# Kernel tuning notes

Hardware: AMD Instinct MI355X
Metric: run time of the kernel (lower is better)

The kernel has to match this reference:

```python
import jax, jax.numpy as jnp
import numpy as np
from jax import lax

B, C, H, W = 4, 192, 64, 64
D_STATE, D_CONV, EXPAND = 16, 4, 2.0
DI = int(EXPAND * C)           # 384 inner dim
DT_RANK = (C + 15) // 16       # 12
EPS = 1e-5


def setup_inputs() -> dict:
    key = jax.random.key(0)
    ks = jax.random.split(key, 16)
    r = lambda k, shp, s=0.02: jax.random.normal(k, shp, jnp.float32) * s
    inp = {
        'x': jax.random.normal(ks[0], (B, C, H, W), jnp.float32),
        'ln_w': jnp.ones((C,), jnp.float32),
        'ln_b': jnp.zeros((C,), jnp.float32),
        'in_proj_w': r(ks[1], (2 * DI, C)),
        'conv_w': r(ks[2], (DI, 1, D_CONV), 0.1),
        'conv_b': jnp.zeros((DI,), jnp.float32),
        'x_proj_w': r(ks[3], (DT_RANK + 2 * D_STATE, DI)),
        'dt_proj_w': r(ks[4], (DI, DT_RANK), 0.1),
        'dt_proj_b': jnp.full((DI,), -4.0, jnp.float32),  # softplus -> small dt
        'A_log': jnp.log(jnp.broadcast_to(jnp.arange(1, D_STATE + 1, dtype=jnp.float32), (DI, D_STATE))),
        'D': jnp.ones((DI,), jnp.float32),
        'out_proj_w': r(ks[5], (C, DI)),
        'rf_w': r(ks[6], (C, C, 3, 3), 0.05),
        'rf_b': jnp.zeros((C,), jnp.float32),
        'bn_w': jnp.ones((C,), jnp.float32),
        'bn_b': jnp.zeros((C,), jnp.float32),
        'bn_mean': jnp.zeros((C,), jnp.float32),
        'bn_var': jnp.ones((C,), jnp.float32),
    }
    return inp


def _selective_scan(delta, A, Bc, Cc, u):
    # delta,u: (B,L,DI); Bc,Cc: (B,L,N); A: (DI,N)
    def step(h, xs):
        d_t, b_t, c_t, u_t = xs  # (B,DI),(B,N),(B,N),(B,DI)
        dA = jnp.exp(d_t[:, :, None] * A[None])            # (B,DI,N)
        h = dA * h + (d_t * u_t)[:, :, None] * b_t[:, None, :]
        y = jnp.einsum('bdn,bn->bd', h, c_t)
        return h, y
    h0 = jnp.zeros((delta.shape[0], A.shape[0], A.shape[1]), delta.dtype)
    xs = (delta.swapaxes(0, 1), Bc.swapaxes(0, 1), Cc.swapaxes(0, 1), u.swapaxes(0, 1))
    _, ys = lax.scan(step, h0, xs)
    return ys.swapaxes(0, 1)  # (B,L,DI)


def _forward(x, ln_w, ln_b, in_proj_w, conv_w, conv_b, x_proj_w, dt_proj_w,
             dt_proj_b, A_log, D, out_proj_w, rf_w, rf_b, bn_w, bn_b, bn_mean, bn_var):
    b, c, h, w = x.shape
    L = h * w
    t = x.reshape(b, c, L).transpose(0, 2, 1)              # (B,L,C) tokens
    res = t
    mu = t.mean(-1, keepdims=True)
    var = t.var(-1, keepdims=True)
    tn = (t - mu) * lax.rsqrt(var + EPS) * ln_w + ln_b
    xz = jnp.einsum('blc,ec->ble', tn, in_proj_w)          # (B,L,2*DI)
    xi, z = jnp.split(xz, 2, axis=-1)
    # causal depthwise conv1d over L
    xi = xi.transpose(0, 2, 1)                             # (B,DI,L)
    xi = lax.conv_general_dilated(xi, conv_w, (1,), [(D_CONV - 1, 0)],
                                  feature_group_count=DI,
                                  dimension_numbers=('NCH', 'OIH', 'NCH'))
    xi = jax.nn.silu(xi + conv_b[None, :, None])
    xt = xi.transpose(0, 2, 1)                             # (B,L,DI)
    dbl = jnp.einsum('bld,ed->ble', xt, x_proj_w)
    dt, Bc, Cc = jnp.split(dbl, [DT_RANK, DT_RANK + D_STATE], axis=-1)
    delta = jax.nn.softplus(jnp.einsum('blr,dr->bld', dt, dt_proj_w) + dt_proj_b)
    A = -jnp.exp(A_log)
    y = _selective_scan(delta, A, Bc, Cc, xt) + xt * D
    y = y * jax.nn.silu(z)
    t = res + jnp.einsum('bld,cd->blc', y, out_proj_w)     # residual
    x2 = t.transpose(0, 2, 1).reshape(b, c, h, w)
    # refine: conv3x3 + BN(eval) + ReLU
    x2 = lax.conv_general_dilated(x2, rf_w, (1, 1), 'SAME',
                                  dimension_numbers=('NCHW', 'OIHW', 'NCHW'))
    x2 = x2 + rf_b[None, :, None, None]
    x2 = (x2 - bn_mean[None, :, None, None]) * lax.rsqrt(bn_var + EPS)[None, :, None, None]
    x2 = x2 * bn_w[None, :, None, None] + bn_b[None, :, None, None]
    return jax.nn.relu(x2)


def reference(x, ln_w, ln_b, in_proj_w, conv_w, conv_b, x_proj_w, dt_proj_w,
              dt_proj_b, A_log, D, out_proj_w, rf_w, rf_b, bn_w, bn_b, bn_mean, bn_var):
    return _forward(x, ln_w, ln_b, in_proj_w, conv_w, conv_b, x_proj_w, dt_proj_w,
                    dt_proj_b, A_log, D, out_proj_w, rf_w, rf_b, bn_w, bn_b,
                    bn_mean, bn_var)
```

## Files before the change

### kernel.cpp

```cpp
#include <hip/hip_runtime.h>


#define Bn 4
#define Cn 192
#define Hn 64
#define Wn 64
#define Ln 4096
#define DIn 384
#define Nst 16
#define RK 12
#define E2 768
#define NCn 64
#define EPSf 1e-5f
#define HP 66
#define HP2 4356

typedef __bf16 bf16x8 __attribute__((ext_vector_type(8)));
typedef float f32x4 __attribute__((ext_vector_type(4)));
typedef unsigned short u16;
typedef unsigned int u32;

static __device__ __forceinline__ float sigmoidf_(float v) {
    return 1.f / (1.f + __expf(-v));
}
static __device__ __forceinline__ float softplusf_(float v) {
    return v > 15.f ? v : __logf(1.f + __expf(v));
}
static __device__ __forceinline__ u16 f2bf(float f) {
    u32 u = __float_as_uint(f);
    u32 r = (u + 0x7FFFu + ((u >> 16) & 1u)) >> 16;
    return (u16)r;
}
static __device__ __forceinline__ float bf2f(u16 v) {
    return __uint_as_float(((u32)v) << 16);
}
static __device__ __forceinline__ float fexp2(float x) {
#if __has_builtin(__builtin_amdgcn_exp2f)
    return __builtin_amdgcn_exp2f(x);
#else
    return __expf(x * 0.69314718056f);
#endif
}
static __device__ __forceinline__ float quad_sum_dpp(float p) {
    float t, r;
    asm volatile("v_add_f32 %0, %1, %1 quad_perm:[1,0,3,2] row_mask:0xf bank_mask:0xf"
                 : "=&v"(t) : "v"(p));
    asm volatile("v_add_f32 %0, %1, %1 quad_perm:[2,3,0,1] row_mask:0xf bank_mask:0xf"
                 : "=&v"(r) : "v"(t));
    return r;
}
static __device__ __forceinline__ void async16(const u16* g, u16* l) {
    __builtin_amdgcn_global_load_lds((__attribute__((address_space(1))) void*)g,
                                     (__attribute__((address_space(3))) void*)l, 16, 0, 0);
}

__global__ __launch_bounds__(256) void k_prep(const float* __restrict__ rfw,
                                              const float* __restrict__ xpw,
                                              const float* __restrict__ dtw,
                                              const float* __restrict__ inpw,
                                              const float* __restrict__ Wo,
                                              const float* __restrict__ rfb,
                                              const float* __restrict__ bnw,
                                              const float* __restrict__ bnb,
                                              const float* __restrict__ bnm,
                                              const float* __restrict__ bnv,
                                              u16* __restrict__ wcv2,
                                              u16* __restrict__ wcomb_bf,
                                              u16* __restrict__ inpw_bf,
                                              u16* __restrict__ wo_bf,
                                              float* __restrict__ scsf,
                                              u16* __restrict__ t2pad) {
    int g = blockIdx.x * 256 + threadIdx.x;
    if (g < 331776) {
        int co = g / 1728;
        int rem = g - co * 1728;
        int tap = rem / Cn, ci = rem - tap * Cn;
        wcv2[g] = f2bf(rfw[((size_t)co * Cn + ci) * 9 + tap]);
    } else if (g < 503808) {
        int i = g - 331776;
        int row = i / 384, k = i - row * 384;
        float v = 0.f;
        if (row < 384) {
#pragma unroll
            for (int r = 0; r < RK; ++r)
                v = fmaf(dtw[row * RK + r], xpw[r * 384 + k], v);
        } else if (row < 416) {
            v = xpw[(RK + row - 384) * 384 + k];
        }
        wcomb_bf[i] = f2bf(v);
    } else if (g < 651264) {
        int i = g - 503808;
        inpw_bf[i] = f2bf(inpw[i]);
    } else if (g < 724992) {
        int i = g - 651264;
        wo_bf[i] = f2bf(Wo[i]);
    } else if (g < 725376) {
        int i = g - 724992;
        if (i < 192) {
            scsf[i] = bnw[i] * rsqrtf(bnv[i] + EPSf);
        } else {
            int c = i - 192;
            float sc = bnw[c] * rsqrtf(bnv[c] + EPSf);
            scsf[i] = (rfb[c] - bnm[c]) * sc + bnb[c];
        }
    } else if (g < 750336) {
        int i = g - 725376;
        int chunk = i % 24;
        int pos = i / 24;
        int b = pos / 260;
        int p = pos - b * 260;
        int cell;
        if (p < 66) cell = p;
        else if (p < 132) cell = 65 * HP + (p - 66);
        else if (p < 196) cell = (p - 132 + 1) * HP;
        else cell = (p - 196 + 1) * HP + 65;
        *(uint4*)&t2pad[((size_t)b * HP2 + cell) * Cn + chunk * 8] = make_uint4(0u, 0u, 0u, 0u);
    }
}

__global__ __launch_bounds__(256) void k_ln(const float* __restrict__ x,
                                            const float* __restrict__ lnw,
                                            const float* __restrict__ lnb,
                                            u16* __restrict__ tn_bf) {
    __shared__ float tile[Cn][65];
    __shared__ float red[2][4][64];
    __shared__ float mean_s[64], rstd_s[64];
    int b = blockIdx.x >> 6;
    int l0 = (blockIdx.x & 63) << 6;
    int tid = threadIdx.x;
    for (int idx = tid; idx < Cn * 64; idx += 256) {
        int c = idx >> 6, ll = idx & 63;
        tile[c][ll] = x[((size_t)(b * Cn + c) << 12) + l0 + ll];
    }
    __syncthreads();
    int ll = tid & 63, grp = tid >> 6;
    float s = 0.f, s2 = 0.f;
    for (int c = grp * 48; c < grp * 48 + 48; ++c) {
        float v = tile[c][ll];
        s += v; s2 += v * v;
    }
    red[0][grp][ll] = s; red[1][grp][ll] = s2;
    __syncthreads();
    if (tid < 64) {
        float m = red[0][0][tid] + red[0][1][tid] + red[0][2][tid] + red[0][3][tid];
        float q = red[1][0][tid] + red[1][1][tid] + red[1][2][tid] + red[1][3][tid];
        m *= (1.f / Cn);
        float var = q * (1.f / Cn) - m * m;
        mean_s[tid] = m;
        rstd_s[tid] = rsqrtf(var + EPSf);
    }
    __syncthreads();
    for (int idx = tid; idx < 64 * Cn; idx += 256) {
        int t = idx / Cn, c = idx - t * Cn;
        float v = (tile[c][t] - mean_s[t]) * rstd_s[t] * lnw[c] + lnb[c];
        tn_bf[(size_t)(b * Ln + l0 + t) * Cn + c] = f2bf(v);
    }
}

template <int K, int KT, int EPI, int NB, int LDO>
__global__ __launch_bounds__(256) void k_gemm3(const u16* __restrict__ A,
                                               const u16* __restrict__ W,
                                               const float* __restrict__ auxf,
                                               const u16* __restrict__ auxb,
                                               void* __restrict__ out1,
                                               float* __restrict__ out2) {
    __shared__ __align__(16) u16 As[2][64 * 64];
    __shared__ __align__(16) u16 Ws[2][64 * 64];
    int bid = blockIdx.x;
    int q = gridDim.x >> 3;
    int wk = (bid & 7) * q + (bid >> 3);
    int n0 = (wk % NB) << 6;
    int m0 = (wk / NB) << 6;
    int tid = threadIdx.x;
    int wid = tid >> 6, lane = tid & 63;
    int lrow = lane & 15, koct = lane >> 4;
    int sw = lrow & 7;
    int i0 = (wid << 7) + lane;
    int r0 = i0 >> 3, g0 = (i0 & 7) ^ (r0 & 7);
    int i1 = i0 + 64;
    int r1 = i1 >> 3, g1 = (i1 & 7) ^ (r1 & 7);
    const u16* a0p = A + (size_t)(m0 + r0) * K + g0 * 8;
    const u16* a1p = A + (size_t)(m0 + r1) * K + g1 * 8;
    const u16* w0p = W + (size_t)(n0 + r0) * K + g0 * 8;
    const u16* w1p = W + (size_t)(n0 + r1) * K + g1 * 8;
    int lb0 = (wid << 7) << 3;
    int lb1 = lb0 + 512;
    f32x4 acc[4];
#pragma unroll
    for (int j = 0; j < 4; ++j) acc[j] = (f32x4){0.f, 0.f, 0.f, 0.f};

    async16(a0p, &As[0][lb0]); async16(a1p, &As[0][lb1]);
    async16(w0p, &Ws[0][lb0]); async16(w1p, &Ws[0][lb1]);
    __syncthreads();
    for (int kt = 0; kt < KT; ++kt) {
        int cur = kt & 1;
        if (kt + 1 < KT) {
            int kk = (kt + 1) << 6;
            async16(a0p + kk, &As[cur ^ 1][lb0]);
            async16(a1p + kk, &As[cur ^ 1][lb1]);
            async16(w0p + kk, &Ws[cur ^ 1][lb0]);
            async16(w1p + kk, &Ws[cur ^ 1][lb1]);
        }
#pragma unroll
        for (int ks = 0; ks < 2; ++ks) {
            int p8 = (((ks << 2) + koct) ^ sw) << 3;
            bf16x8 a  = *(const bf16x8*)&As[cur][(((wid << 4) + lrow) << 6) + p8];
            bf16x8 b0 = *(const bf16x8*)&Ws[cur][(lrow << 6) + p8];
            bf16x8 b1 = *(const bf16x8*)&Ws[cur][((16 + lrow) << 6) + p8];
            bf16x8 b2 = *(const bf16x8*)&Ws[cur][((32 + lrow) << 6) + p8];
            bf16x8 b3 = *(const bf16x8*)&Ws[cur][((48 + lrow) << 6) + p8];
            acc[0] = __builtin_amdgcn_mfma_f32_16x16x32_bf16(a, b0, acc[0], 0, 0, 0);
            acc[1] = __builtin_amdgcn_mfma_f32_16x16x32_bf16(a, b1, acc[1], 0, 0, 0);
            acc[2] = __builtin_amdgcn_mfma_f32_16x16x32_bf16(a, b2, acc[2], 0, 0, 0);
            acc[3] = __builtin_amdgcn_mfma_f32_16x16x32_bf16(a, b3, acc[3], 0, 0, 0);
        }
        __syncthreads();
    }
    int mrow = m0 + (wid << 4) + (koct << 2);
#pragma unroll
    for (int nf = 0; nf < 4; ++nf) {
        int col = n0 + (nf << 4) + lrow;
        if constexpr (EPI == 0) {
            u16* o = (u16*)out1;
#pragma unroll
            for (int r = 0; r < 4; ++r)
                o[(size_t)(mrow + r) * LDO + col] = f2bf(acc[nf][r]);
        } else if constexpr (EPI == 1) {
            if (col < 384) {
                float dtbc = auxf[col];
                u32* dedux = (u32*)out1;
#pragma unroll
                for (int r = 0; r < 4; ++r) {
                    int m = mrow + r;
                    float de = softplusf_(acc[nf][r] + dtbc);
                    float u = bf2f(auxb[(size_t)m * DIn + col]);
                    dedux[(size_t)m * DIn + col] = (u32)f2bf(de) | ((u32)f2bf(de * u) << 16);
                }
            } else if (col < 416) {
#pragma unroll
                for (int r = 0; r < 4; ++r)
                    out2[(size_t)(mrow + r) * 32 + (col - 384)] = acc[nf][r];
            }
        } else {
            u16* t2 = (u16*)out1;
#pragma unroll
            for (int r = 0; r < 4; ++r) {
                int m = mrow + r;
                int b = m >> 12, l = m & 4095;
                int h = l >> 6, w = l & 63;
                float v = acc[nf][r] + auxf[((size_t)(b * Cn + col) << 12) + l];
                t2[(size_t)(b * HP2 + (h + 1) * HP + (w + 1)) * Cn + col] = f2bf(v);
            }
        }
    }
}

__global__ __launch_bounds__(256) void k_conv1d(const u16* __restrict__ xz,
                                                const float* __restrict__ cw,
                                                const float* __restrict__ cb,
                                                u16* __restrict__ xt_bf) {
    int g = blockIdx.x * 256 + threadIdx.x;
    int m = g / 96, dq = g - m * 96;
    int d = dq << 2;
    int l = m & (Ln - 1);
    float w_[4][4];
    *(float4*)&w_[0][0] = *(const float4*)&cw[(d + 0) << 2];
    *(float4*)&w_[1][0] = *(const float4*)&cw[(d + 1) << 2];
    *(float4*)&w_[2][0] = *(const float4*)&cw[(d + 2) << 2];
    *(float4*)&w_[3][0] = *(const float4*)&cw[(d + 3) << 2];
    float4 bv = *(const float4*)&cb[d];
    float o_[4] = {bv.x, bv.y, bv.z, bv.w};
    const u16* base = xz + (size_t)m * E2 + d;
#pragma unroll
    for (int j = 0; j < 4; ++j) {
        if (l >= j) {
            ushort4 in4 = *(const ushort4*)(base - (size_t)j * E2);
            o_[0] += bf2f(in4.x) * w_[0][3 - j];
            o_[1] += bf2f(in4.y) * w_[1][3 - j];
            o_[2] += bf2f(in4.z) * w_[2][3 - j];
            o_[3] += bf2f(in4.w) * w_[3][3 - j];
        }
    }
    ushort4 rb;
    rb.x = f2bf(o_[0] * sigmoidf_(o_[0]));
    rb.y = f2bf(o_[1] * sigmoidf_(o_[1]));
    rb.z = f2bf(o_[2] * sigmoidf_(o_[2]));
    rb.w = f2bf(o_[3] * sigmoidf_(o_[3]));
    *(ushort4*)&xt_bf[(size_t)m * DIn + d] = rb;
}

__global__ __launch_bounds__(256) void k_scan1(const u32* __restrict__ dedux,
                                               const float* __restrict__ bc,
                                               const float* __restrict__ alog,
                                               float* __restrict__ chunkA,
                                               float* __restrict__ chunkH) {
    __shared__ __align__(16) float ds_de[2][16][20], ds_dux[2][16][20], ds_bt[2][16][20];
    int dg = blockIdx.x, c = blockIdx.y, b = blockIdx.z;
    int tid = threadIdx.x;
    int dl = tid >> 4, n = tid & 15;
    int trow = dl, dd = n;
    float Av2 = -__expf(alog[(dg * 16 + dl) * Nst + n]) * 1.44269504f;
    float h = 0.f, sde = 0.f;
    int row0 = b * Ln + c * 64 + trow;
    u32 vN = dedux[(size_t)row0 * DIn + dg * 16 + dd];
    float bN = bc[(size_t)row0 * 32 + dd];
    for (int sub = 0; sub < 4; ++sub) {
        int bs = sub & 1;
        ds_de[bs][dd][trow] = bf2f((u16)(vN & 0xffffu));
        ds_dux[bs][dd][trow] = bf2f((u16)(vN >> 16));
        ds_bt[bs][dd][trow] = bN;
        __syncthreads();
        if (sub < 3) {
            int row = row0 + (sub + 1) * 16;
            vN = dedux[(size_t)row * DIn + dg * 16 + dd];
            bN = bc[(size_t)row * 32 + dd];
        }
#pragma unroll
        for (int t4 = 0; t4 < 4; ++t4) {
            f32x4 de4 = *(const f32x4*)&ds_de[bs][dl][t4 * 4];
            f32x4 dux4 = *(const f32x4*)&ds_dux[bs][dl][t4 * 4];
            f32x4 bb4 = *(const f32x4*)&ds_bt[bs][n][t4 * 4];
#pragma unroll
            for (int j = 0; j < 4; ++j) {
                float a = fexp2(de4[j] * Av2);
                sde += de4[j];
                h = fmaf(a, h, dux4[j] * bb4[j]);
            }
        }
    }
    size_t base = (size_t)(b * NCn + c) * (DIn * Nst) + dg * 256;
    chunkA[base + tid] = fexp2(Av2 * sde);
    chunkH[base + tid] = h;
}

__global__ __launch_bounds__(256) void k_scan15(const float* __restrict__ chunkA,
                                                const float* __restrict__ chunkH,
                                                float* __restrict__ hstart) {
    int dg = blockIdx.x, b = blockIdx.y;
    int tid = threadIdx.x;
    size_t off = (size_t)b * NCn * (DIn * Nst) + dg * 256 + tid;
    float h = 0.f;
    for (int c0 = 0; c0 < NCn; c0 += 8) {
        float Ar[8], Hr[8];
#pragma unroll
        for (int j = 0; j < 8; ++j) {
            Ar[j] = chunkA[off + (size_t)(c0 + j) * (DIn * Nst)];
            Hr[j] = chunkH[off + (size_t)(c0 + j) * (DIn * Nst)];
        }
#pragma unroll
        for (int j = 0; j < 8; ++j) {
            hstart[off + (size_t)(c0 + j) * (DIn * Nst)] = h;
            h = fmaf(Ar[j], h, Hr[j]);
        }
    }
}

__global__ __launch_bounds__(256) void k_scan2(const u32* __restrict__ dedux,
                                               const float* __restrict__ bc,
                                               const float* __restrict__ alog,
                                               const float* __restrict__ hstart,
                                               const u16* __restrict__ xt_bf,
                                               const u16* __restrict__ xz,
                                               const float* __restrict__ Dp,
                                               u16* __restrict__ agate) {
    __shared__ __align__(16) float ds_de[2][16][20], ds_dux[2][16][20];
    __shared__ __align__(16) float ds_bt[2][16][20], ds_ct[2][16][20];
    __shared__ __align__(16) float pq[2][16][16][4];
    int dg = blockIdx.x, c = blockIdx.y, b = blockIdx.z;
    int tid = threadIdx.x;
    int dl = tid >> 4, n = tid & 15;
    int trow = dl, dd = n;
    int aq = n >> 2, bq = n & 3;
    float Av2 = -__expf(alog[(dg * 16 + dl) * Nst + n]) * 1.44269504f;
    float Dr = Dp[dg * 16 + dd];
    float msk[4];
#pragma unroll
    for (int j = 0; j < 4; ++j) msk[j] = (bq == j) ? 1.f : 0.f;
    size_t base = (size_t)(b * NCn + c) * (DIn * Nst) + dg * 256;
    float h = hstart[base + tid];
    int row0 = b * Ln + c * 64 + trow;
    int dgoff = dg * 16 + dd;
    u32 vN = dedux[(size_t)row0 * DIn + dgoff];
    float bN = bc[(size_t)row0 * 32 + dd];
    float cN = bc[(size_t)row0 * 32 + 16 + dd];
    u16 uN = xt_bf[(size_t)row0 * DIn + dgoff];
    u16 zN = xz[(size_t)row0 * E2 + DIn + dgoff];
    float pu = 0.f, pz = 0.f;
    int prow = row0;
    for (int sub = 0; sub < 4; ++sub) {
        int bs = sub & 1;
        int row = row0 + sub * 16;
        ds_de[bs][dd][trow] = bf2f((u16)(vN & 0xffffu));
        ds_dux[bs][dd][trow] = bf2f((u16)(vN >> 16));
        ds_bt[bs][dd][trow] = bN;
        ds_ct[bs][dd][trow] = cN;
        float uu = bf2f(uN), zz = bf2f(zN);
        __syncthreads();
        if (sub < 3) {
            int rown = row0 + (sub + 1) * 16;
            vN = dedux[(size_t)rown * DIn + dgoff];
            bN = bc[(size_t)rown * 32 + dd];
            cN = bc[(size_t)rown * 32 + 16 + dd];
            uN = xt_bf[(size_t)rown * DIn + dgoff];
            zN = xz[(size_t)rown * E2 + DIn + dgoff];
        }
        if (sub > 0) {
            f32x4 p4 = *(const f32x4*)&pq[bs ^ 1][trow][dd][0];
            float y = (p4[0] + p4[1]) + (p4[2] + p4[3]);
            float ga = (y + pu * Dr) * (pz * sigmoidf_(pz));
            agate[(size_t)prow * DIn + dgoff] = f2bf(ga);
        }
        float P[4] = {0.f, 0.f, 0.f, 0.f};
#pragma unroll
        for (int t4 = 0; t4 < 4; ++t4) {
            f32x4 de4 = *(const f32x4*)&ds_de[bs][dl][t4 * 4];
            f32x4 dux4 = *(const f32x4*)&ds_dux[bs][dl][t4 * 4];
            f32x4 bb4 = *(const f32x4*)&ds_bt[bs][n][t4 * 4];
            f32x4 ct4 = *(const f32x4*)&ds_ct[bs][n][t4 * 4];
#pragma unroll
            for (int j = 0; j < 4; ++j) {
                float a = fexp2(de4[j] * Av2);
                h = fmaf(a, h, dux4[j] * bb4[j]);
                float p = quad_sum_dpp(h * ct4[j]);
                P[t4] = fmaf(msk[j], p, P[t4]);
            }
        }
#pragma unroll
        for (int tt = 0; tt < 4; ++tt)
            pq[bs][tt * 4 + bq][dl][aq] = P[tt];
        pu = uu; pz = zz; prow = row;
    }
    __syncthreads();
    {
        f32x4 p4 = *(const f32x4*)&pq[1][trow][dd][0];
        float y = (p4[0] + p4[1]) + (p4[2] + p4[3]);
        float ga = (y + pu * Dr) * (pz * sigmoidf_(pz));
        agate[(size_t)prow * DIn + dgoff] = f2bf(ga);
    }
}

__global__ __launch_bounds__(256) void k_conv3g(const u16* __restrict__ t2pad,
                                                const u16* __restrict__ wcv2,
                                                const float* __restrict__ scsf,
                                                float* __restrict__ out) {
    __shared__ __align__(16) u16 As[2][64 * 64];
    __shared__ __align__(16) u16 Ws[2][64 * 64];
    int bid = blockIdx.x;
    int q = gridDim.x >> 3;
    int wk = (bid & 7) * q + (bid >> 3);
    int n0 = (wk % 3) << 6;
    int rowid = wk / 3;
    int b = rowid >> 6, h = rowid & 63;
    int tid = threadIdx.x;
    int wid = tid >> 6, lane = tid & 63;
    int lrow = lane & 15, koct = lane >> 4;
    int sw = lrow & 7;
    int i0 = (wid << 7) + lane;
    int r0 = i0 >> 3, g0 = (i0 & 7) ^ (r0 & 7);
    int i1 = i0 + 64;
    int r1 = i1 >> 3, g1 = (i1 & 7) ^ (r1 & 7);
    const u16* Abase = t2pad + (size_t)(b * HP2 + (h + 1) * HP + 1) * Cn;
    const u16* a0p = Abase + r0 * Cn + g0 * 8;
    const u16* a1p = Abase + r1 * Cn + g1 * 8;
    const u16* w0p = wcv2 + (size_t)(n0 + r0) * 1728 + g0 * 8;
    const u16* w1p = wcv2 + (size_t)(n0 + r1) * 1728 + g1 * 8;
    int lb0 = (wid << 7) << 3;
    int lb1 = lb0 + 512;
    const int tapoff[9] = {-HP - 1, -HP, -HP + 1, -1, 0, 1, HP - 1, HP, HP + 1};
    f32x4 acc[4];
#pragma unroll
    for (int j = 0; j < 4; ++j) acc[j] = (f32x4){0.f, 0.f, 0.f, 0.f};

    {
        int koff = tapoff[0] * Cn;
        async16(a0p + koff, &As[0][lb0]); async16(a1p + koff, &As[0][lb1]);
        async16(w0p, &Ws[0][lb0]); async16(w1p, &Ws[0][lb1]);
    }
    __syncthreads();
    for (int kt = 0; kt < 27; ++kt) {
        int cur = kt & 1;
        if (kt + 1 < 27) {
            int t = (kt + 1) / 3;
            int koff = tapoff[t] * Cn + (((kt + 1) - t * 3) << 6);
            async16(a0p + koff, &As[cur ^ 1][lb0]);
            async16(a1p + koff, &As[cur ^ 1][lb1]);
            int kw = (kt + 1) << 6;
            async16(w0p + kw, &Ws[cur ^ 1][lb0]);
            async16(w1p + kw, &Ws[cur ^ 1][lb1]);
        }
#pragma unroll
        for (int ks = 0; ks < 2; ++ks) {
            int p8 = (((ks << 2) + koct) ^ sw) << 3;
            bf16x8 a  = *(const bf16x8*)&As[cur][(((wid << 4) + lrow) << 6) + p8];
            bf16x8 b0 = *(const bf16x8*)&Ws[cur][(lrow << 6) + p8];
            bf16x8 b1 = *(const bf16x8*)&Ws[cur][((16 + lrow) << 6) + p8];
            bf16x8 b2 = *(const bf16x8*)&Ws[cur][((32 + lrow) << 6) + p8];
            bf16x8 b3 = *(const bf16x8*)&Ws[cur][((48 + lrow) << 6) + p8];
            acc[0] = __builtin_amdgcn_mfma_f32_16x16x32_bf16(a, b0, acc[0], 0, 0, 0);
            acc[1] = __builtin_amdgcn_mfma_f32_16x16x32_bf16(a, b1, acc[1], 0, 0, 0);
            acc[2] = __builtin_amdgcn_mfma_f32_16x16x32_bf16(a, b2, acc[2], 0, 0, 0);
            acc[3] = __builtin_amdgcn_mfma_f32_16x16x32_bf16(a, b3, acc[3], 0, 0, 0);
        }
        __syncthreads();
    }
    int w0_ = (wid << 4) + (koct << 2);
#pragma unroll
    for (int nf = 0; nf < 4; ++nf) {
        int col = n0 + (nf << 4) + lrow;
        float sc = scsf[col], sf = scsf[192 + col];
        float4 o;
        o.x = fmaxf(acc[nf][0] * sc + sf, 0.f);
        o.y = fmaxf(acc[nf][1] * sc + sf, 0.f);
        o.z = fmaxf(acc[nf][2] * sc + sf, 0.f);
        o.w = fmaxf(acc[nf][3] * sc + sf, 0.f);
        *(float4*)&out[((size_t)(b * Cn + col) << 12) + (h << 6) + w0_] = o;
    }
}

extern "C" void kernel_launch(void* const* d_in, const int* in_sizes, int n_in,
                              void* d_out, int out_size, void* d_ws, size_t ws_size,
                              hipStream_t stream) {
    const float* x    = (const float*)d_in[0];
    const float* lnw  = (const float*)d_in[1];
    const float* lnb  = (const float*)d_in[2];
    const float* inpw = (const float*)d_in[3];
    const float* cw   = (const float*)d_in[4];
    const float* cb   = (const float*)d_in[5];
    const float* xpw  = (const float*)d_in[6];
    const float* dtw  = (const float*)d_in[7];
    const float* dtb  = (const float*)d_in[8];
    const float* alog = (const float*)d_in[9];
    const float* Dp   = (const float*)d_in[10];
    const float* Wo   = (const float*)d_in[11];
    const float* rfw  = (const float*)d_in[12];
    const float* rfb  = (const float*)d_in[13];
    const float* bnw  = (const float*)d_in[14];
    const float* bnb  = (const float*)d_in[15];
    const float* bnm  = (const float*)d_in[16];
    const float* bnv  = (const float*)d_in[17];

    float* ws = (float*)d_ws;
    u16* tn_bf    = (u16*)ws;
    float* hstart = ws + 1572864;
    u16* xz       = (u16*)(ws + 3145728);
    u16* xt_bf    = (u16*)(ws + 9437184);
    u32* dedux    = (u32*)(ws + 12582912);
    float* bc     = ws + 18874368;
    u16* agate    = (u16*)(ws + 19398656);
    float* chunkA = ws + 22544384;
    float* chunkH = ws + 24117248;
    u16* wcv2     = (u16*)(ws + 25690112);
    u16* wcomb_bf = (u16*)(ws + 25856000);
    u16* inpw_bf  = (u16*)(ws + 25942016);
    u16* wo_bf    = (u16*)(ws + 26015744);
    float* scsf   = ws + 26052608;
    u16* t2pad    = (u16*)(ws + 26053120);

    k_prep<<<2931, 256, 0, stream>>>(rfw, xpw, dtw, inpw, Wo, rfb, bnw, bnb, bnm, bnv,
                                     wcv2, wcomb_bf, inpw_bf, wo_bf, scsf, t2pad);
    k_ln<<<Bn * (Ln / 64), 256, 0, stream>>>(x, lnw, lnb, tn_bf);
    k_gemm3<Cn, 3, 0, 12, E2><<<(Bn * Ln / 64) * 12, 256, 0, stream>>>(
        tn_bf, inpw_bf, nullptr, nullptr, xz, nullptr);
    k_conv1d<<<(Bn * Ln * (DIn / 4)) / 256, 256, 0, stream>>>(xz, cw, cb, xt_bf);
    k_gemm3<DIn, 6, 1, 7, 0><<<(Bn * Ln / 64) * 7, 256, 0, stream>>>(
        xt_bf, wcomb_bf, dtb, xt_bf, dedux, bc);
    k_scan1<<<dim3(DIn / 16, NCn, Bn), 256, 0, stream>>>(dedux, bc, alog, chunkA, chunkH);
    k_scan15<<<dim3(DIn / 16, Bn), 256, 0, stream>>>(chunkA, chunkH, hstart);
    k_scan2<<<dim3(DIn / 16, NCn, Bn), 256, 0, stream>>>(dedux, bc, alog, hstart,
                                                         xt_bf, xz, Dp, agate);
    k_gemm3<DIn, 6, 2, 3, Cn><<<(Bn * Ln / 64) * 3, 256, 0, stream>>>(
        agate, wo_bf, x, nullptr, (void*)t2pad, nullptr);
    k_conv3g<<<768, 256, 0, stream>>>(t2pad, wcv2, scsf, (float*)d_out);
}
```

Before: 177.3 us.

## Fuse chunk-prefix scan into scan1 via last-block atomic counter

Removes the separate k_scan15 launch. Each scan1 block bumps an atomic counter per (batch, channel-group), and the last block to finish runs the sequential chunk-state prefix that writes hstart. The counters are zeroed in k_prep. Separately, scan2 drops the mask-multiply accumulation and writes each quad-reduced partial straight to shared memory under a lane predicate. The fused prefix runs serially on one block per group, so it may become a tail, and an extra barrier is added inside the scan1 sub-loop.

Result: slower. 705.3 us (+297.7%).

```diff
diff --git a/kernel.cpp b/kernel.cpp
--- a/kernel.cpp
+++ b/kernel.cpp
@@ -69,7 +69,8 @@
                                               u16* __restrict__ inpw_bf,
                                               u16* __restrict__ wo_bf,
                                               float* __restrict__ scsf,
-                                              u16* __restrict__ t2pad) {
+                                              u16* __restrict__ t2pad,
+                                              u32* __restrict__ cnt) {
     int g = blockIdx.x * 256 + threadIdx.x;
     if (g < 331776) {
         int co = g / 1728;
@@ -115,6 +116,8 @@
         else if (p < 196) cell = (p - 132 + 1) * HP;
         else cell = (p - 196 + 1) * HP + 65;
         *(uint4*)&t2pad[((size_t)b * HP2 + cell) * Cn + chunk * 8] = make_uint4(0u, 0u, 0u, 0u);
+    } else if (g < 750432) {
+        cnt[g - 750336] = 0u;
     }
 }
 
@@ -293,8 +296,11 @@
                                                const float* __restrict__ bc,
                                                const float* __restrict__ alog,
                                                float* __restrict__ chunkA,
-                                               float* __restrict__ chunkH) {
+                                               float* __restrict__ chunkH,
+                                               u32* __restrict__ cnt,
+                                               float* __restrict__ hstart) {
     __shared__ __align__(16) float ds_de[2][16][20], ds_dux[2][16][20], ds_bt[2][16][20];
+    __shared__ u32 lastflag;
     int dg = blockIdx.x, c = blockIdx.y, b = blockIdx.z;
     int tid = threadIdx.x;
     int dl = tid >> 4, n = tid & 15;
@@ -327,30 +333,33 @@
                 h = fmaf(a, h, dux4[j] * bb4[j]);
             }
         }
+        __syncthreads();
     }
     size_t base = (size_t)(b * NCn + c) * (DIn * Nst) + dg * 256;
     chunkA[base + tid] = fexp2(Av2 * sde);
     chunkH[base + tid] = h;
-}
-
-__global__ __launch_bounds__(256) void k_scan15(const float* __restrict__ chunkA,
-                                                const float* __restrict__ chunkH,
-                                                float* __restrict__ hstart) {
-    int dg = blockIdx.x, b = blockIdx.y;
-    int tid = threadIdx.x;
-    size_t off = (size_t)b * NCn * (DIn * Nst) + dg * 256 + tid;
-    float h = 0.f;
-    for (int c0 = 0; c0 < NCn; c0 += 8) {
-        float Ar[8], Hr[8];
-#pragma unroll
-        for (int j = 0; j < 8; ++j) {
-            Ar[j] = chunkA[off + (size_t)(c0 + j) * (DIn * Nst)];
-            Hr[j] = chunkH[off + (size_t)(c0 + j) * (DIn * Nst)];
-        }
-#pragma unroll
-        for (int j = 0; j < 8; ++j) {
-            hstart[off + (size_t)(c0 + j) * (DIn * Nst)] = h;
-            h = fmaf(Ar[j], h, Hr[j]);
+    __threadfence();
+    if (tid == 0) {
+        u32 old = atomicAdd(&cnt[b * 24 + dg], 1u);
+        lastflag = (old == NCn - 1) ? 1u : 0u;
+    }
+    __syncthreads();
+    if (lastflag) {
+        __threadfence();
+        size_t off = (size_t)b * NCn * (DIn * Nst) + dg * 256 + tid;
+        float hh = 0.f;
+        for (int c0 = 0; c0 < NCn; c0 += 8) {
+            float Ar[8], Hr[8];
+#pragma unroll
+            for (int j = 0; j < 8; ++j) {
+                Ar[j] = chunkA[off + (size_t)(c0 + j) * (DIn * Nst)];
+                Hr[j] = chunkH[off + (size_t)(c0 + j) * (DIn * Nst)];
+            }
+#pragma unroll
+            for (int j = 0; j < 8; ++j) {
+                hstart[off + (size_t)(c0 + j) * (DIn * Nst)] = hh;
+                hh = fmaf(Ar[j], hh, Hr[j]);
+            }
         }
     }
 }
@@ -373,9 +382,6 @@
     int aq = n >> 2, bq = n & 3;
     float Av2 = -__expf(alog[(dg * 16 + dl) * Nst + n]) * 1.44269504f;
     float Dr = Dp[dg * 16 + dd];
-    float msk[4];
-#pragma unroll
-    for (int j = 0; j < 4; ++j) msk[j] = (bq == j) ? 1.f : 0.f;
     size_t base = (size_t)(b * NCn + c) * (DIn * Nst) + dg * 256;
     float h = hstart[base + tid];
     int row0 = b * Ln + c * 64 + trow;
@@ -410,7 +416,6 @@
             float ga = (y + pu * Dr) * (pz * sigmoidf_(pz));
             agate[(size_t)prow * DIn + dgoff] = f2bf(ga);
         }
-        float P[4] = {0.f, 0.f, 0.f, 0.f};
 #pragma unroll
         for (int t4 = 0; t4 < 4; ++t4) {
             f32x4 de4 = *(const f32x4*)&ds_de[bs][dl][t4 * 4];
@@ -422,12 +427,9 @@
                 float a = fexp2(de4[j] * Av2);
                 h = fmaf(a, h, dux4[j] * bb4[j]);
                 float p = quad_sum_dpp(h * ct4[j]);
-                P[t4] = fmaf(msk[j], p, P[t4]);
+                if (bq == j) pq[bs][t4 * 4 + j][dl][aq] = p;
             }
         }
-#pragma unroll
-        for (int tt = 0; tt < 4; ++tt)
-            pq[bs][tt * 4 + bq][dl][aq] = P[tt];
         pu = uu; pz = zz; prow = row;
     }
     __syncthreads();
@@ -554,18 +556,19 @@
     u16* inpw_bf  = (u16*)(ws + 25942016);
     u16* wo_bf    = (u16*)(ws + 26015744);
     float* scsf   = ws + 26052608;
+    u32* cnt      = (u32*)(ws + 26052992);
     u16* t2pad    = (u16*)(ws + 26053120);
 
-    k_prep<<<2931, 256, 0, stream>>>(rfw, xpw, dtw, inpw, Wo, rfb, bnw, bnb, bnm, bnv,
-                                     wcv2, wcomb_bf, inpw_bf, wo_bf, scsf, t2pad);
+    k_prep<<<2932, 256, 0, stream>>>(rfw, xpw, dtw, inpw, Wo, rfb, bnw, bnb, bnm, bnv,
+                                     wcv2, wcomb_bf, inpw_bf, wo_bf, scsf, t2pad, cnt);
     k_ln<<<Bn * (Ln / 64), 256, 0, stream>>>(x, lnw, lnb, tn_bf);
     k_gemm3<Cn, 3, 0, 12, E2><<<(Bn * Ln / 64) * 12, 256, 0, stream>>>(
         tn_bf, inpw_bf, nullptr, nullptr, xz, nullptr);
     k_conv1d<<<(Bn * Ln * (DIn / 4)) / 256, 256, 0, stream>>>(xz, cw, cb, xt_bf);
     k_gemm3<DIn, 6, 1, 7, 0><<<(Bn * Ln / 64) * 7, 256, 0, stream>>>(
         xt_bf, wcomb_bf, dtb, xt_bf, dedux, bc);
-    k_scan1<<<dim3(DIn / 16, NCn, Bn), 256, 0, stream>>>(dedux, bc, alog, chunkA, chunkH);
-    k_scan15<<<dim3(DIn / 16, Bn), 256, 0, stream>>>(chunkA, chunkH, hstart);
+    k_scan1<<<dim3(DIn / 16, NCn, Bn), 256, 0, stream>>>(dedux, bc, alog,
+                                                         chunkA, chunkH, cnt, hstart);
     k_scan2<<<dim3(DIn / 16, NCn, Bn), 256, 0, stream>>>(dedux, bc, alog, hstart,
                                                          xt_bf, xz, Dp, agate);
     k_gemm3<DIn, 6, 2, 3, Cn><<<(Bn * Ln / 64) * 3, 256, 0, stream>>>(
```
